# Performance work log

Measured on AMD Instinct MI355X. Metric: run time of the kernel, lower is better.

## Reference

```python
import jax, jax.numpy as jnp
import numpy as np

N, E, D, H = 50000, 500000, 128, 4
FH = D // H  # per-head dim of gat1
NEG_SLOPE = 0.2
EPS = 1e-16  # PyG softmax denominator epsilon


def _gat_layer(x, src, dst, W, a_src, a_dst, bias, heads, fh):
    # W: [D_in, heads*fh]; a_src/a_dst: [heads, fh]; bias: [heads*fh]
    n = x.shape[0]
    xp = (x @ W).reshape(n, heads, fh)                     # [N,H,F]
    alpha_s = jnp.einsum('nhf,hf->nh', xp, a_src)          # [N,H]
    alpha_d = jnp.einsum('nhf,hf->nh', xp, a_dst)
    e = alpha_s[src] + alpha_d[dst]                        # [E,H]
    e = jnp.where(e > 0, e, NEG_SLOPE * e)                 # leaky_relu
    # edge softmax grouped by destination node
    m = jax.lax.stop_gradient(jax.ops.segment_max(e, dst, num_segments=n))
    a = jnp.exp(e - m[dst])
    denom = jax.ops.segment_sum(a, dst, num_segments=n)
    a = a / (denom[dst] + EPS)                             # [E,H]
    msg = a[:, :, None] * xp[src]                          # [E,H,F]
    out = jax.ops.segment_sum(msg, dst, num_segments=n)    # [N,H,F]
    return out.reshape(n, heads * fh) + bias


def setup_inputs() -> dict:
    key = jax.random.key(0)
    ks = jax.random.split(key, 20)

    def glorot(k, shape):
        fan_in, fan_out = shape[0], shape[-1]
        std = (2.0 / (fan_in + fan_out)) ** 0.5
        return std * jax.random.normal(k, shape, dtype=jnp.float32)

    inp = {
        'x': jax.random.normal(ks[0], (N, 1), dtype=jnp.float32),
        'edge_index': jax.random.randint(ks[1], (E, 2), 0, N, dtype=jnp.int64 if jax.config.jax_enable_x64 else jnp.int32),
        'W_emb': glorot(ks[2], (1, D)),   # nn.Linear(1, d_node), stored as [in,out]
        'b_emb': jnp.zeros((D,), jnp.float32),
        # gat1: in=D, heads=H, per-head out=FH
        'W1': glorot(ks[3], (D, H * FH)),
        'as1': glorot(ks[4], (H, FH)),
        'ad1': glorot(ks[5], (H, FH)),
        'b1': jnp.zeros((H * FH,), jnp.float32),
        # gat2/3/4: in=D, heads=1, out=D
        'W2': glorot(ks[6], (D, D)), 'as2': glorot(ks[7], (1, D)), 'ad2': glorot(ks[8], (1, D)), 'b2': jnp.zeros((D,), jnp.float32),
        'W3': glorot(ks[9], (D, D)), 'as3': glorot(ks[10], (1, D)), 'ad3': glorot(ks[11], (1, D)), 'b3': jnp.zeros((D,), jnp.float32),
        'W4': glorot(ks[12], (D, D)), 'as4': glorot(ks[13], (1, D)), 'ad4': glorot(ks[14], (1, D)), 'b4': jnp.zeros((D,), jnp.float32),
    }
    return inp


def reference(x, edge_index, W_emb, b_emb, W1, as1, ad1, b1,
              W2, as2, ad2, b2, W3, as3, ad3, b3, W4, as4, ad4, b4):
    # emb: Linear(1 -> D)
    h = x @ W_emb + b_emb                                  # [N,D]
    # edge_index.t(): row 0 = src, row 1 = dst; GATConv adds self-loops
    loop = jnp.arange(N, dtype=edge_index.dtype)
    src = jnp.concatenate([edge_index[:, 0], loop])
    dst = jnp.concatenate([edge_index[:, 1], loop])
    h = jax.nn.relu(_gat_layer(h, src, dst, W1, as1, ad1, b1, H, FH))
    h = jax.nn.relu(_gat_layer(h, src, dst, W2, as2, ad2, b2, 1, D))
    h = jax.nn.relu(_gat_layer(h, src, dst, W3, as3, ad3, b3, 1, D))
    h = _gat_layer(h, src, dst, W4, as4, ad4, b4, 1, D)
    return h
```

## Files before the change

kernel.cpp:

```cpp
#include <hip/hip_runtime.h>
#include <math.h>


#define LEAKY(e) ((e) > 0.f ? (e) : 0.2f * (e))

typedef __attribute__((ext_vector_type(8))) short bf16x8;
typedef __attribute__((ext_vector_type(4))) float f32x4;

__device__ inline ushort f32_to_bf16_rne(float f) {
    unsigned u = __float_as_uint(f);
    unsigned r = (u + 0x7FFFu + ((u >> 16) & 1u)) >> 16;
    return (ushort)r;
}
__device__ inline float bf16_to_f32(ushort h) { return __uint_as_float((unsigned)h << 16); }
__device__ inline unsigned pack2(float a, float b) {
    return (unsigned)f32_to_bf16_rne(a) | ((unsigned)f32_to_bf16_rne(b) << 16);
}


__global__ void k_scatterpad(const int* __restrict__ ei, int E, int N,
                             int* __restrict__ deg, int* __restrict__ csr_pad,
                             int2* __restrict__ ovf, int ovf_cap) {
    int e = blockIdx.x * blockDim.x + threadIdx.x;
    int Et = E + N;
    if (e >= Et) return;
    int src, dst;
    if (e < E) { int2 p = ((const int2*)ei)[e]; src = p.x; dst = p.y; }
    else { src = dst = e - E; }
    int pos = atomicAdd(&deg[dst], 1);
    if (pos < 64) {
        csr_pad[(dst << 6) + pos] = src;
    } else {
        int o = atomicAdd(&deg[N], 1);
        if (o < ovf_cap) ovf[o] = make_int2(dst, src);
    }
}


__global__ void k_prep(const float* __restrict__ Wa, const float* __restrict__ Wb,
                       const float* __restrict__ Wc,
                       const float* __restrict__ asa, const float* __restrict__ asb,
                       const float* __restrict__ asc,
                       const float* __restrict__ ada, const float* __restrict__ adb,
                       const float* __restrict__ adc,
                       const float* __restrict__ W_emb, const float* __restrict__ b_emb,
                       const float* __restrict__ W1g, const float* __restrict__ as1g,
                       const float* __restrict__ ad1g,
                       ushort* __restrict__ hi0, ushort* __restrict__ lo0,
                       ushort* __restrict__ hi1, ushort* __restrict__ lo1,
                       ushort* __restrict__ hi2, ushort* __restrict__ lo2,
                       float* __restrict__ was0, float* __restrict__ was1,
                       float* __restrict__ was2,
                       float* __restrict__ wad0, float* __restrict__ wad1,
                       float* __restrict__ wad2,
                       float* __restrict__ consts) {
    __shared__ float su[128], sv[128];
    int b = blockIdx.x, tid = threadIdx.x;
    if (b < 192) {
        int l = b >> 6;
        int idx = (b & 63) * 256 + tid;
        const float* W = (l == 0) ? Wa : (l == 1) ? Wb : Wc;
        ushort* ph = (l == 0) ? hi0 : (l == 1) ? hi1 : hi2;
        ushort* pl = (l == 0) ? lo0 : (l == 1) ? lo1 : lo2;
        int k = idx >> 7, c = idx & 127;
        float w = W[idx];
        ushort hi = f32_to_bf16_rne(w);
        ushort lo = f32_to_bf16_rne(w - bf16_to_f32(hi));
        ph[c * 128 + k] = hi;
        pl[c * 128 + k] = lo;
    } else if (b < 195) {
        if (tid >= 128) return;
        int l = b - 192;
        const float* W  = (l == 0) ? Wa : (l == 1) ? Wb : Wc;
        const float* av = (l == 0) ? asa : (l == 1) ? asb : asc;
        const float* dv = (l == 0) ? ada : (l == 1) ? adb : adc;
        float* ws = (l == 0) ? was0 : (l == 1) ? was1 : was2;
        float* wd = (l == 0) ? wad0 : (l == 1) ? wad1 : wad2;
        int k = tid;
        float s = 0.f, d = 0.f;
        for (int c = 0; c < 128; c++) {
            float w = W[k * 128 + c];
            s += w * av[c];
            d += w * dv[c];
        }
        ws[k] = s; wd[k] = d;
    } else {
        if (tid >= 128) return;
        int f = tid;
        float u = 0.f, v = 0.f;
        for (int k = 0; k < 128; k++) {
            u += W_emb[k] * W1g[k * 128 + f];
            v += b_emb[k] * W1g[k * 128 + f];
        }
        su[f] = u; sv[f] = v;
        consts[f] = u; consts[128 + f] = v;
        __syncthreads();
        if (f < 4) {
            float P = 0.f, Q = 0.f, R = 0.f, S = 0.f;
            for (int j = 0; j < 32; j++) {
                float uu = su[f * 32 + j], vv = sv[f * 32 + j];
                float a = as1g[f * 32 + j], d = ad1g[f * 32 + j];
                P += uu * a; Q += vv * a; R += uu * d; S += vv * d;
            }
            consts[256 + f] = P; consts[260 + f] = Q;
            consts[264 + f] = R; consts[268 + f] = S;
        }
    }
}

__global__ __launch_bounds__(256) void k_l1(const float* __restrict__ x,
        const int* __restrict__ deg, const int* __restrict__ csr_pad,
        const int2* __restrict__ ovf,
        const float* __restrict__ consts, const float* __restrict__ b1,
        const float* __restrict__ was2, const float* __restrict__ wad2,
        float* __restrict__ hout, float* __restrict__ a_s, float* __restrict__ a_d,
        int n) {
    int w = threadIdx.x >> 6, lane = threadIdx.x & 63;
    int node = blockIdx.x * 4 + w;
    if (node >= n) return;
    int q = lane & 3;
    int el = lane >> 2;
    float P = consts[256 + q], Q = consts[260 + q];
    float R = consts[264 + q], Sc = consts[268 + q];
    float xd = x[node];
    float c0 = xd * R + Sc + Q;
    int dg = deg[node];
    int dlim = min(dg, 64);
    float den = 0.f, S = 0.f;
    for (int i = el; i < dlim; i += 16) {
        float xs = x[csr_pad[(node << 6) + i]];
        float e = xs * P + c0;
        e = LEAKY(e);
        float wgt = __expf(e);
        den += wgt;
        S += wgt * xs;
    }
    if (dg > 64) {
        int no = deg[n];
        for (int i = el; i < no; i += 16) {
            int2 p = ovf[i];
            if (p.x == node) {
                float xs = x[p.y];
                float e = xs * P + c0;
                e = LEAKY(e);
                float wgt = __expf(e);
                den += wgt;
                S += wgt * xs;
            }
        }
    }
#pragma unroll
    for (int off = 4; off < 64; off <<= 1) {
        den += __shfl_xor(den, off, 64);
        S += __shfl_xor(S, off, 64);
    }
    float inv = 1.f / (den + 1e-16f);
    float Sn = S * inv, Swn = den * inv;
    int f = q * 32 + el * 2;
    float2 u  = *(const float2*)(consts + f);
    float2 v  = *(const float2*)(consts + 128 + f);
    float2 bb = *(const float2*)(b1 + f);
    float2 ws = *(const float2*)(was2 + f);
    float2 wd = *(const float2*)(wad2 + f);
    float v0 = fmaxf(Sn * u.x + Swn * v.x + bb.x, 0.f);
    float v1 = fmaxf(Sn * u.y + Swn * v.y + bb.y, 0.f);
    *(float2*)(hout + (size_t)node * 128 + f) = make_float2(v0, v1);
    float ps = v0 * ws.x + v1 * ws.y;
    float pd = v0 * wd.x + v1 * wd.y;
#pragma unroll
    for (int off = 1; off < 64; off <<= 1) {
        ps += __shfl_xor(ps, off, 64);
        pd += __shfl_xor(pd, off, 64);
    }
    if (lane == 0) { a_s[node] = ps; a_d[node] = pd; }
}

__global__ __launch_bounds__(256) void k_aggh(const float* __restrict__ h,
        const float* __restrict__ as, const float* __restrict__ ad,
        const int* __restrict__ deg, const int* __restrict__ csr_pad,
        const int2* __restrict__ ovf,
        unsigned* __restrict__ aggp, int n) {
    __shared__ int2 s_sw[4][64];
    int w = threadIdx.x >> 6, lane = threadIdx.x & 63;
    int node = blockIdx.x * 4 + w;
    if (node >= n) return;
    int dg = deg[node];
    float adval = ad[node];
    const char* hbase = (const char*)h;

    if (dg <= 64) {
        int boff = 0;
        float e = -INFINITY;
        if (lane < dg) {
            int src = csr_pad[(node << 6) + lane];
            boff = src << 9;
            e = LEAKY(as[src] + adval);
        }
        float m = e;
#pragma unroll
        for (int off = 32; off > 0; off >>= 1) m = fmaxf(m, __shfl_xor(m, off, 64));
        float wt = (lane < dg) ? __expf(e - m) : 0.f;
        float den = wt;
#pragma unroll
        for (int off = 32; off > 0; off >>= 1) den += __shfl_xor(den, off, 64);
        s_sw[w][lane] = make_int2(boff, __float_as_int(wt));
        __builtin_amdgcn_wave_barrier();

        int half = lane >> 5;
        int q16 = (lane & 31) * 16;
        float4 acc = make_float4(0.f, 0.f, 0.f, 0.f);
        int degp = (dg + 7) & ~7;
        for (int j = 0; j < degp; j += 8) {
#pragma unroll
            for (int t = 0; t < 4; t++) {
                int2 p = s_sw[w][j + 2 * t + half];
                float4 v = *(const float4*)(hbase + p.x + q16);
                float wt2 = __int_as_float(p.y);
                acc.x += wt2 * v.x; acc.y += wt2 * v.y;
                acc.z += wt2 * v.z; acc.w += wt2 * v.w;
            }
        }
        acc.x += __shfl_xor(acc.x, 32, 64);
        acc.y += __shfl_xor(acc.y, 32, 64);
        acc.z += __shfl_xor(acc.z, 32, 64);
        acc.w += __shfl_xor(acc.w, 32, 64);
        float inv = 1.f / (den + 1e-16f);
        if (lane < 32) {
            float o0 = acc.x * inv, o1 = acc.y * inv;
            float o2 = acc.z * inv, o3 = acc.w * inv;
            ushort h0 = f32_to_bf16_rne(o0), h1 = f32_to_bf16_rne(o1);
            ushort h2 = f32_to_bf16_rne(o2), h3 = f32_to_bf16_rne(o3);
            uint4 pk;
            pk.x = (unsigned)h0 | ((unsigned)h1 << 16);
            pk.y = pack2(o0 - bf16_to_f32(h0), o1 - bf16_to_f32(h1));
            pk.z = (unsigned)h2 | ((unsigned)h3 << 16);
            pk.w = pack2(o2 - bf16_to_f32(h2), o3 - bf16_to_f32(h3));
            ((uint4*)aggp)[(size_t)node * 32 + lane] = pk;
        }
    } else {
        int lane8 = lane * 8;
        int no = deg[n];
        int psrc = csr_pad[(node << 6) + lane];
        float m = LEAKY(as[psrc] + adval);
        for (int i = lane; i < no; i += 64) {
            int2 p = ovf[i];
            if (p.x == node) m = fmaxf(m, LEAKY(as[p.y] + adval));
        }
#pragma unroll
        for (int off = 32; off > 0; off >>= 1) m = fmaxf(m, __shfl_xor(m, off, 64));
        float den = 0.f;
        float2 acc = make_float2(0.f, 0.f);
        for (int i = 0; i < 64; i++) {
            int src = csr_pad[(node << 6) + i];
            float e = LEAKY(as[src] + adval);
            float wt = __expf(e - m);
            den += wt;
            float2 v = *(const float2*)(hbase + ((size_t)src << 9) + lane8);
            acc.x += wt * v.x; acc.y += wt * v.y;
        }
        for (int i = 0; i < no; i++) {
            int2 p = ovf[i];
            if (p.x == node) {
                float e = LEAKY(as[p.y] + adval);
                float wt = __expf(e - m);
                den += wt;
                float2 v = *(const float2*)(hbase + ((size_t)p.y << 9) + lane8);
                acc.x += wt * v.x; acc.y += wt * v.y;
            }
        }
        float inv = 1.f / (den + 1e-16f);
        float o0 = acc.x * inv, o1 = acc.y * inv;
        ushort h0 = f32_to_bf16_rne(o0), h1 = f32_to_bf16_rne(o1);
        ((uint2*)aggp)[(size_t)node * 64 + lane] =
            make_uint2((unsigned)h0 | ((unsigned)h1 << 16),
                       pack2(o0 - bf16_to_f32(h0), o1 - bf16_to_f32(h1)));
    }
}

__global__ __launch_bounds__(512) void k_gemm(const uint2* __restrict__ aggp,
        const ushort* __restrict__ wt_hi, const ushort* __restrict__ wt_lo,
        const float* __restrict__ bias, float* __restrict__ hout,
        const float* __restrict__ was_nx, const float* __restrict__ wad_nx,
        float* __restrict__ as_nx, float* __restrict__ ad_nx,
        int n, int do_relu) {
    __shared__ ushort Bh[16 * 128 * 8];
    __shared__ ushort Bl[16 * 128 * 8];
    int tid = threadIdx.x;
#pragma unroll
    for (int rep = 0; rep < 4; rep++) {
        int c = rep * 512 + tid;
        int col = c >> 4, kc = c & 15;
        *(uint4*)(Bh + (size_t)(kc * 128 + col) * 8) = *(const uint4*)(wt_hi + (size_t)col * 128 + kc * 8);
        *(uint4*)(Bl + (size_t)(kc * 128 + col) * 8) = *(const uint4*)(wt_lo + (size_t)col * 128 + kc * 8);
    }

    int wid = tid >> 6, lane = tid & 63;
    int lrow = lane & 15, kgrp = lane >> 4;
    int row_base = blockIdx.x * 128 + wid * 16;
    int arow = min(row_base + lrow, n - 1);

    const uint4* ap = (const uint4*)(aggp + (size_t)arow * 64);
    uint4 qa[8];
#pragma unroll
    for (int ks = 0; ks < 4; ks++) {
        qa[2 * ks]     = ap[ks * 8 + kgrp * 2];
        qa[2 * ks + 1] = ap[ks * 8 + kgrp * 2 + 1];
    }
    __syncthreads();

    f32x4 acc[8];
#pragma unroll
    for (int nn = 0; nn < 8; nn++) { acc[nn][0] = 0.f; acc[nn][1] = 0.f; acc[nn][2] = 0.f; acc[nn][3] = 0.f; }

#pragma unroll
    for (int ks = 0; ks < 4; ks++) {
        uint4 q0 = qa[2 * ks], q1 = qa[2 * ks + 1];
        int4 hi4 = make_int4(q0.x, q0.z, q1.x, q1.z);
        int4 lo4 = make_int4(q0.y, q0.w, q1.y, q1.w);
        bf16x8 ah = *(bf16x8*)&hi4;
        bf16x8 al = *(bf16x8*)&lo4;
        int kc = ks * 4 + kgrp;
#pragma unroll
        for (int nn = 0; nn < 8; nn++) {
            int col = nn * 16 + lrow;
            bf16x8 bh = *(const bf16x8*)(Bh + (size_t)(kc * 128 + col) * 8);
            bf16x8 bl = *(const bf16x8*)(Bl + (size_t)(kc * 128 + col) * 8);
            acc[nn] = __builtin_amdgcn_mfma_f32_16x16x32_bf16(ah, bh, acc[nn], 0, 0, 0);
            acc[nn] = __builtin_amdgcn_mfma_f32_16x16x32_bf16(ah, bl, acc[nn], 0, 0, 0);
            acc[nn] = __builtin_amdgcn_mfma_f32_16x16x32_bf16(al, bh, acc[nn], 0, 0, 0);
        }
    }

    float bv[8], wsv[8], wdv[8];
#pragma unroll
    for (int nn = 0; nn < 8; nn++) bv[nn] = bias[nn * 16 + lrow];
    if (was_nx) {
#pragma unroll
        for (int nn = 0; nn < 8; nn++) {
            wsv[nn] = was_nx[nn * 16 + lrow];
            wdv[nn] = wad_nx[nn * 16 + lrow];
        }
    }

#pragma unroll
    for (int i = 0; i < 4; i++) {
        int row = row_base + kgrp * 4 + i;
        if (row < n) {
            float ps = 0.f, pd = 0.f;
#pragma unroll
            for (int nn = 0; nn < 8; nn++) {
                float val = acc[nn][i] + bv[nn];
                if (do_relu) val = fmaxf(val, 0.f);
                hout[(size_t)row * 128 + nn * 16 + lrow] = val;
                if (was_nx) { ps += val * wsv[nn]; pd += val * wdv[nn]; }
            }
            if (was_nx) {
#pragma unroll
                for (int off = 1; off < 16; off <<= 1) {
                    ps += __shfl_xor(ps, off, 16);
                    pd += __shfl_xor(pd, off, 16);
                }
                if (lrow == 0) { as_nx[row] = ps; ad_nx[row] = pd; }
            }
        }
    }
}


extern "C" void kernel_launch(void* const* d_in, const int* in_sizes, int n_in,
                              void* d_out, int out_size, void* d_ws, size_t ws_size,
                              hipStream_t stream) {
    const float* x     = (const float*)d_in[0];
    const int*   ei    = (const int*)d_in[1];
    const float* W_emb = (const float*)d_in[2];
    const float* b_emb = (const float*)d_in[3];
    const float* W1g   = (const float*)d_in[4];
    const float* as1g  = (const float*)d_in[5];
    const float* ad1g  = (const float*)d_in[6];
    const float* b1    = (const float*)d_in[7];
    const float* Wl[3]  = {(const float*)d_in[8],  (const float*)d_in[12], (const float*)d_in[16]};
    const float* asl[3] = {(const float*)d_in[9],  (const float*)d_in[13], (const float*)d_in[17]};
    const float* adl[3] = {(const float*)d_in[10], (const float*)d_in[14], (const float*)d_in[18]};
    const float* bl[3]  = {(const float*)d_in[11], (const float*)d_in[15], (const float*)d_in[19]};
    float* out = (float*)d_out;

    int N = in_sizes[0];
    int E = in_sizes[1] / 2;
    int Et = E + N;
    const int OVF_CAP = 65536;

    char* ws = (char*)d_ws;
    size_t off = 0;
    auto alloc = [&](size_t bytes) { size_t p = off; off += (bytes + 255) & ~(size_t)255; return p; };
    int*   deg      = (int*)(ws + alloc((size_t)(N + 1) * 4));
    int2*  ovf      = (int2*)(ws + alloc((size_t)OVF_CAP * 8));
    int*   csr_pad  = (int*)(ws + alloc((size_t)N * 64 * 4));
    float* consts   = (float*)(ws + alloc(272 * 4));
    float* a_s0     = (float*)(ws + alloc((size_t)N * 4));
    float* a_d0     = (float*)(ws + alloc((size_t)N * 4));
    float* a_s1     = (float*)(ws + alloc((size_t)N * 4));
    float* a_d1     = (float*)(ws + alloc((size_t)N * 4));
    float* hA       = (float*)(ws + alloc((size_t)N * 128 * 4));
    unsigned* aggp  = (unsigned*)(ws + alloc((size_t)N * 64 * 8));
    ushort* wt_hi[3]; ushort* wt_lo[3];
    float* was[3]; float* wad[3];
    for (int l = 0; l < 3; l++) {
        wt_hi[l] = (ushort*)(ws + alloc(128 * 128 * 2));
        wt_lo[l] = (ushort*)(ws + alloc(128 * 128 * 2));
        was[l]   = (float*)(ws + alloc(128 * 4));
        wad[l]   = (float*)(ws + alloc(128 * 4));
    }

    hipMemsetAsync(deg, 0, (size_t)(N + 1) * 4, stream);
    k_scatterpad<<<(Et + 255) / 256, 256, 0, stream>>>(ei, E, N, deg, csr_pad,
                                                       ovf, OVF_CAP);
    k_prep<<<196, 256, 0, stream>>>(Wl[0], Wl[1], Wl[2], asl[0], asl[1], asl[2],
                                    adl[0], adl[1], adl[2],
                                    W_emb, b_emb, W1g, as1g, ad1g,
                                    wt_hi[0], wt_lo[0], wt_hi[1], wt_lo[1], wt_hi[2], wt_lo[2],
                                    was[0], was[1], was[2], wad[0], wad[1], wad[2],
                                    consts);

    k_l1<<<(N + 3) / 4, 256, 0, stream>>>(x, deg, csr_pad, ovf, consts, b1,
                                          was[0], wad[0], hA, a_s0, a_d0, N);

    float* as_cur = a_s0; float* ad_cur = a_d0;
    float* as_nxt = a_s1; float* ad_nxt = a_d1;
    for (int l = 0; l < 3; l++) {
        k_aggh<<<(N + 3) / 4, 256, 0, stream>>>(hA, as_cur, ad_cur, deg, csr_pad,
                                                ovf, aggp, N);
        if (l < 2) {
            k_gemm<<<(N + 127) / 128, 512, 0, stream>>>((const uint2*)aggp, wt_hi[l], wt_lo[l], bl[l], hA,
                                                        was[l + 1], wad[l + 1], as_nxt, ad_nxt, N, 1);
            float* t;
            t = as_cur; as_cur = as_nxt; as_nxt = t;
            t = ad_cur; ad_cur = ad_nxt; ad_nxt = t;
        } else {
            k_gemm<<<(N + 127) / 128, 512, 0, stream>>>((const uint2*)aggp, wt_hi[l], wt_lo[l], bl[l], out,
                                                        nullptr, nullptr, nullptr, nullptr, N, 0);
        }
    }
}
```

Measured before the change: 247.4 us.

## Pre-swizzle weights into MFMA fragment layout and read from global, fuse init kernels

Weights are now stored in MFMA B-fragment order at prep time, so the GEMM kernel loads its B operands directly from global/L2 instead of staging the whole weight matrix in LDS and synchronising. The GEMM block size drops from 512 to 256 threads with 64 rows per block. The scatter and prep kernels are merged into a single launch to save one kernel launch. The trade-off is repeated global/L2 weight reads per wave instead of shared LDS reuse.

```diff
diff --git a/kernel.cpp b/kernel.cpp
--- a/kernel.cpp
+++ b/kernel.cpp
@@ -18,26 +18,10 @@
 }
 
 
-__global__ void k_scatterpad(const int* __restrict__ ei, int E, int N,
-                             int* __restrict__ deg, int* __restrict__ csr_pad,
-                             int2* __restrict__ ovf, int ovf_cap) {
-    int e = blockIdx.x * blockDim.x + threadIdx.x;
-    int Et = E + N;
-    if (e >= Et) return;
-    int src, dst;
-    if (e < E) { int2 p = ((const int2*)ei)[e]; src = p.x; dst = p.y; }
-    else { src = dst = e - E; }
-    int pos = atomicAdd(&deg[dst], 1);
-    if (pos < 64) {
-        csr_pad[(dst << 6) + pos] = src;
-    } else {
-        int o = atomicAdd(&deg[N], 1);
-        if (o < ovf_cap) ovf[o] = make_int2(dst, src);
-    }
-}
-
-
-__global__ void k_prep(const float* __restrict__ Wa, const float* __restrict__ Wb,
+__global__ void k_init(const int* __restrict__ ei, int E, int N, int nScat,
+                       int* __restrict__ deg, int* __restrict__ csr_pad,
+                       int2* __restrict__ ovf, int ovf_cap,
+                       const float* __restrict__ Wa, const float* __restrict__ Wb,
                        const float* __restrict__ Wc,
                        const float* __restrict__ asa, const float* __restrict__ asb,
                        const float* __restrict__ asc,
@@ -55,7 +39,24 @@
                        float* __restrict__ wad2,
                        float* __restrict__ consts) {
     __shared__ float su[128], sv[128];
-    int b = blockIdx.x, tid = threadIdx.x;
+    int blk = blockIdx.x, tid = threadIdx.x;
+    if (blk < nScat) {
+        int e = blk * 256 + tid;
+        int Et = E + N;
+        if (e >= Et) return;
+        int src, dst;
+        if (e < E) { int2 p = ((const int2*)ei)[e]; src = p.x; dst = p.y; }
+        else { src = dst = e - E; }
+        int pos = atomicAdd(&deg[dst], 1);
+        if (pos < 64) {
+            csr_pad[(dst << 6) + pos] = src;
+        } else {
+            int o = atomicAdd(&deg[N], 1);
+            if (o < ovf_cap) ovf[o] = make_int2(dst, src);
+        }
+        return;
+    }
+    int b = blk - nScat;
     if (b < 192) {
         int l = b >> 6;
         int idx = (b & 63) * 256 + tid;
@@ -66,8 +67,11 @@
         float w = W[idx];
         ushort hi = f32_to_bf16_rne(w);
         ushort lo = f32_to_bf16_rne(w - bf16_to_f32(hi));
-        ph[c * 128 + k] = hi;
-        pl[c * 128 + k] = lo;
+        int ks = k >> 5, kgrp = (k >> 3) & 3, j = k & 7;
+        int nn = c >> 4, lrow = c & 15;
+        int off = (((ks * 8 + nn) * 64) + kgrp * 16 + lrow) * 8 + j;
+        ph[off] = hi;
+        pl[off] = lo;
     } else if (b < 195) {
         if (tid >= 128) return;
         int l = b - 192;
@@ -277,68 +281,49 @@
     }
 }
 
-__global__ __launch_bounds__(512) void k_gemm(const uint2* __restrict__ aggp,
-        const ushort* __restrict__ wt_hi, const ushort* __restrict__ wt_lo,
+__global__ __launch_bounds__(256) void k_gemm(const uint2* __restrict__ aggp,
+        const ushort* __restrict__ wf_hi, const ushort* __restrict__ wf_lo,
         const float* __restrict__ bias, float* __restrict__ hout,
         const float* __restrict__ was_nx, const float* __restrict__ wad_nx,
         float* __restrict__ as_nx, float* __restrict__ ad_nx,
         int n, int do_relu) {
-    __shared__ ushort Bh[16 * 128 * 8];
-    __shared__ ushort Bl[16 * 128 * 8];
-    int tid = threadIdx.x;
-#pragma unroll
-    for (int rep = 0; rep < 4; rep++) {
-        int c = rep * 512 + tid;
-        int col = c >> 4, kc = c & 15;
-        *(uint4*)(Bh + (size_t)(kc * 128 + col) * 8) = *(const uint4*)(wt_hi + (size_t)col * 128 + kc * 8);
-        *(uint4*)(Bl + (size_t)(kc * 128 + col) * 8) = *(const uint4*)(wt_lo + (size_t)col * 128 + kc * 8);
-    }
-
-    int wid = tid >> 6, lane = tid & 63;
+    int tid = threadIdx.x, wid = tid >> 6, lane = tid & 63;
     int lrow = lane & 15, kgrp = lane >> 4;
-    int row_base = blockIdx.x * 128 + wid * 16;
+    int row_base = blockIdx.x * 64 + wid * 16;
     int arow = min(row_base + lrow, n - 1);
-
     const uint4* ap = (const uint4*)(aggp + (size_t)arow * 64);
-    uint4 qa[8];
+
+    float bv[8], wsv[8], wdv[8];
+#pragma unroll
+    for (int nn = 0; nn < 8; nn++) bv[nn] = bias[nn * 16 + lrow];
+    if (was_nx) {
+#pragma unroll
+        for (int nn = 0; nn < 8; nn++) {
+            wsv[nn] = was_nx[nn * 16 + lrow];
+            wdv[nn] = wad_nx[nn * 16 + lrow];
+        }
+    }
+
+    f32x4 acc[8];
+#pragma unroll
+    for (int nn = 0; nn < 8; nn++) { acc[nn][0] = 0.f; acc[nn][1] = 0.f; acc[nn][2] = 0.f; acc[nn][3] = 0.f; }
+
 #pragma unroll
     for (int ks = 0; ks < 4; ks++) {
-        qa[2 * ks]     = ap[ks * 8 + kgrp * 2];
-        qa[2 * ks + 1] = ap[ks * 8 + kgrp * 2 + 1];
-    }
-    __syncthreads();
-
-    f32x4 acc[8];
-#pragma unroll
-    for (int nn = 0; nn < 8; nn++) { acc[nn][0] = 0.f; acc[nn][1] = 0.f; acc[nn][2] = 0.f; acc[nn][3] = 0.f; }
-
-#pragma unroll
-    for (int ks = 0; ks < 4; ks++) {
-        uint4 q0 = qa[2 * ks], q1 = qa[2 * ks + 1];
+        uint4 q0 = ap[ks * 8 + kgrp * 2];
+        uint4 q1 = ap[ks * 8 + kgrp * 2 + 1];
         int4 hi4 = make_int4(q0.x, q0.z, q1.x, q1.z);
         int4 lo4 = make_int4(q0.y, q0.w, q1.y, q1.w);
         bf16x8 ah = *(bf16x8*)&hi4;
         bf16x8 al = *(bf16x8*)&lo4;
-        int kc = ks * 4 + kgrp;
 #pragma unroll
         for (int nn = 0; nn < 8; nn++) {
-            int col = nn * 16 + lrow;
-            bf16x8 bh = *(const bf16x8*)(Bh + (size_t)(kc * 128 + col) * 8);
-            bf16x8 bl = *(const bf16x8*)(Bl + (size_t)(kc * 128 + col) * 8);
+            size_t boff = ((size_t)(ks * 8 + nn) * 64 + lane) * 8;
+            bf16x8 bh = *(const bf16x8*)(wf_hi + boff);
+            bf16x8 bl = *(const bf16x8*)(wf_lo + boff);
             acc[nn] = __builtin_amdgcn_mfma_f32_16x16x32_bf16(ah, bh, acc[nn], 0, 0, 0);
             acc[nn] = __builtin_amdgcn_mfma_f32_16x16x32_bf16(ah, bl, acc[nn], 0, 0, 0);
             acc[nn] = __builtin_amdgcn_mfma_f32_16x16x32_bf16(al, bh, acc[nn], 0, 0, 0);
-        }
-    }
-
-    float bv[8], wsv[8], wdv[8];
-#pragma unroll
-    for (int nn = 0; nn < 8; nn++) bv[nn] = bias[nn * 16 + lrow];
-    if (was_nx) {
-#pragma unroll
-        for (int nn = 0; nn < 8; nn++) {
-            wsv[nn] = was_nx[nn * 16 + lrow];
-            wdv[nn] = wad_nx[nn * 16 + lrow];
         }
     }
 
@@ -388,6 +373,7 @@
     int E = in_sizes[1] / 2;
     int Et = E + N;
     const int OVF_CAP = 65536;
+    int nScat = (Et + 255) / 256;
 
     char* ws = (char*)d_ws;
     size_t off = 0;
@@ -402,24 +388,24 @@
     float* a_d1     = (float*)(ws + alloc((size_t)N * 4));
     float* hA       = (float*)(ws + alloc((size_t)N * 128 * 4));
     unsigned* aggp  = (unsigned*)(ws + alloc((size_t)N * 64 * 8));
-    ushort* wt_hi[3]; ushort* wt_lo[3];
+    ushort* wf_hi[3]; ushort* wf_lo[3];
     float* was[3]; float* wad[3];
     for (int l = 0; l < 3; l++) {
-        wt_hi[l] = (ushort*)(ws + alloc(128 * 128 * 2));
-        wt_lo[l] = (ushort*)(ws + alloc(128 * 128 * 2));
+        wf_hi[l] = (ushort*)(ws + alloc(128 * 128 * 2));
+        wf_lo[l] = (ushort*)(ws + alloc(128 * 128 * 2));
         was[l]   = (float*)(ws + alloc(128 * 4));
         wad[l]   = (float*)(ws + alloc(128 * 4));
     }
 
     hipMemsetAsync(deg, 0, (size_t)(N + 1) * 4, stream);
-    k_scatterpad<<<(Et + 255) / 256, 256, 0, stream>>>(ei, E, N, deg, csr_pad,
-                                                       ovf, OVF_CAP);
-    k_prep<<<196, 256, 0, stream>>>(Wl[0], Wl[1], Wl[2], asl[0], asl[1], asl[2],
-                                    adl[0], adl[1], adl[2],
-                                    W_emb, b_emb, W1g, as1g, ad1g,
-                                    wt_hi[0], wt_lo[0], wt_hi[1], wt_lo[1], wt_hi[2], wt_lo[2],
-                                    was[0], was[1], was[2], wad[0], wad[1], wad[2],
-                                    consts);
+    k_init<<<nScat + 196, 256, 0, stream>>>(ei, E, N, nScat, deg, csr_pad, ovf, OVF_CAP,
+                                            Wl[0], Wl[1], Wl[2], asl[0], asl[1], asl[2],
+                                            adl[0], adl[1], adl[2],
+                                            W_emb, b_emb, W1g, as1g, ad1g,
+                                            wf_hi[0], wf_lo[0], wf_hi[1], wf_lo[1],
+                                            wf_hi[2], wf_lo[2],
+                                            was[0], was[1], was[2], wad[0], wad[1], wad[2],
+                                            consts);
 
     k_l1<<<(N + 3) / 4, 256, 0, stream>>>(x, deg, csr_pad, ovf, consts, b1,
                                           was[0], wad[0], hA, a_s0, a_d0, N);
@@ -430,14 +416,14 @@
         k_aggh<<<(N + 3) / 4, 256, 0, stream>>>(hA, as_cur, ad_cur, deg, csr_pad,
                                                 ovf, aggp, N);
         if (l < 2) {
-            k_gemm<<<(N + 127) / 128, 512, 0, stream>>>((const uint2*)aggp, wt_hi[l], wt_lo[l], bl[l], hA,
-                                                        was[l + 1], wad[l + 1], as_nxt, ad_nxt, N, 1);
+            k_gemm<<<(N + 63) / 64, 256, 0, stream>>>((const uint2*)aggp, wf_hi[l], wf_lo[l], bl[l], hA,
+                                                      was[l + 1], wad[l + 1], as_nxt, ad_nxt, N, 1);
             float* t;
             t = as_cur; as_cur = as_nxt; as_nxt = t;
             t = ad_cur; ad_cur = ad_nxt; ad_nxt = t;
         } else {
-            k_gemm<<<(N + 127) / 128, 512, 0, stream>>>((const uint2*)aggp, wt_hi[l], wt_lo[l], bl[l], out,
-                                                        nullptr, nullptr, nullptr, nullptr, N, 0);
-        }
-    }
-}
+            k_gemm<<<(N + 63) / 64, 256, 0, stream>>>((const uint2*)aggp, wf_hi[l], wf_lo[l], bl[l], out,
+                                                      nullptr, nullptr, nullptr, nullptr, N, 0);
+        }
+    }
+}
```

After: 272.1 us. 1.1x slower.
